# Kernel optimization log

Hardware: AMD Instinct MI355X
Metric: run time of the kernel (lower is better)

## Reference

```python
import jax, jax.numpy as jnp
import numpy as np

VX, VY = 0.16, 0.16
X_OFF = VX / 2 + 0.0          # vx/2 + point_cloud_range[0]
Y_OFF = VY / 2 + (-39.68)     # vy/2 + point_cloud_range[1]
BN_EPS = 1e-3


def setup_inputs() -> dict:
    key = jax.random.key(0)
    P, N, C_IN, C_OUT = 40000, 32, 9, 64
    k1, k2, k3, k4, k5, k6 = jax.random.split(key, 6)
    voxels = jax.random.normal(k1, (P, N, 4), dtype=jnp.float32)
    # at least 1 real point per pillar (avoids div-by-zero, matches real data)
    voxel_num_points = jax.random.randint(k2, (P,), 1, N + 1, dtype=jnp.int32)
    # coords layout: [batch_idx, z, y, x]
    voxel_coords = jax.random.randint(k3, (P, 4), 0, 432, dtype=jnp.int32)
    W = jax.random.normal(k4, (C_OUT, C_IN), dtype=jnp.float32) * 0.1  # 1x1 conv kernel
    gamma = jnp.ones((C_OUT,), jnp.float32)
    beta = jnp.zeros((C_OUT,), jnp.float32)
    running_mean = jax.random.normal(k5, (C_OUT,), jnp.float32) * 0.01
    running_var = jax.random.uniform(k6, (C_OUT,), jnp.float32, minval=0.5, maxval=1.5)
    return {
        "voxels": voxels,
        "W": W,
        "gamma": gamma,
        "beta": beta,
        "running_mean": running_mean,
        "running_var": running_var,
        "voxel_num_points": voxel_num_points,
        "voxel_coords": voxel_coords,
    }


def reference(voxels, W, gamma, beta, running_mean, running_var,
              voxel_num_points, voxel_coords):
    P, N, _ = voxels.shape
    npts = voxel_num_points.astype(voxels.dtype)[:, None, None]          # [P,1,1]
    points_mean = voxels[:, :, :3].sum(axis=1, keepdims=True) / npts     # [P,1,3]
    f_cluster = voxels[:, :, :3] - points_mean                           # [P,N,3]

    cx = voxel_coords[:, 3].astype(voxels.dtype)[:, None] * VX + X_OFF   # [P,1]
    cy = voxel_coords[:, 2].astype(voxels.dtype)[:, None] * VY + Y_OFF
    x_c = voxels[:, :, 0] - cx                                           # [P,N]
    y_c = voxels[:, :, 1] - cy

    # NOTE: torch code mutates features[:,:,:2] in place via the f_center view,
    # so the first two feature channels are ALSO the centered coordinates.
    feats = jnp.concatenate(
        [x_c[..., None], y_c[..., None], voxels[:, :, 2:4],
         f_cluster, x_c[..., None], y_c[..., None]], axis=-1)            # [P,N,9]

    mask = (jnp.arange(N)[None, :] < voxel_num_points[:, None]).astype(voxels.dtype)
    feats = feats * mask[..., None]

    # PFNLayer: 1x1 conv (no bias) + BatchNorm (eval) + ReLU + max over points
    x = jnp.einsum('pnc,oc->pno', feats, W)                              # [P,N,64]
    scale = gamma / jnp.sqrt(running_var + BN_EPS)
    x = (x - running_mean) * scale + beta
    x = jax.nn.relu(x)
    return x.max(axis=1)                                                 # [P,64] pillar_features
```

## Files before the change

### kernel.cpp

```cpp
#include <hip/hip_runtime.h>
#include <cstdint>


__global__ __launch_bounds__(64) void pillar_setup_kernel(
    const float* __restrict__ Wp,
    const float* __restrict__ gamma_p,
    const float* __restrict__ beta_p,
    const float* __restrict__ rmean_p,
    const float* __restrict__ rvar_p,
    float*       __restrict__ params)
{
    const int o = threadIdx.x;
    float w[9];
    #pragma unroll
    for (int c = 0; c < 9; ++c) w[c] = Wp[o * 9 + c];
    const float s = gamma_p[o] / sqrtf(rvar_p[o] + 1e-3f);

    params[0 * 64 + o] = (w[0] + w[4] + w[7]) * s;
    params[1 * 64 + o] = (w[1] + w[5] + w[8]) * s;
    params[2 * 64 + o] = (w[2] + w[6]) * s;
    params[3 * 64 + o] = w[3] * s;
    params[4 * 64 + o] = beta_p[o] - rmean_p[o] * s;
    params[5 * 64 + o] = (w[0] + w[7]) * s;
    params[6 * 64 + o] = (w[1] + w[8]) * s;
    params[7 * 64 + o] = w[4] * s;
    params[8 * 64 + o] = w[5] * s;
    params[9 * 64 + o] = w[6] * s;
}

__global__ __launch_bounds__(256) void pillar_vfe_kernel(
    const float4* __restrict__ voxels4,
    const float*  __restrict__ params,
    const int*    __restrict__ npts_p,
    const int*    __restrict__ coords_p,
    float*        __restrict__ out,
    int P)
{
    __shared__ float4 sh[4 * 32];

    const int tid    = threadIdx.x;
    const int pblock = blockIdx.x * 4;

    if (tid < 128) {
        const int gidx = pblock * 32 + tid;
        if (gidx < P * 32) sh[tid] = voxels4[gidx];
    }
    __syncthreads();

    const int wave = tid >> 6;
    const int lane = tid & 63;
    const int p    = pblock + wave;
    if (p >= P) return;

    const float A0   = params[0 * 64 + lane];
    const float A1   = params[1 * 64 + lane];
    const float A2   = params[2 * 64 + lane];
    const float A3   = params[3 * 64 + lane];
    const float C0   = params[4 * 64 + lane];
    const float SW07 = params[5 * 64 + lane];
    const float SW18 = params[6 * 64 + lane];
    const float SW4  = params[7 * 64 + lane];
    const float SW5  = params[8 * 64 + lane];
    const float SW6  = params[9 * 64 + lane];

    const int   npts = npts_p[p];
    const float fn   = (float)npts;
    const float cx   = (float)coords_p[p * 4 + 3] * 0.16f + 0.08f;
    const float cy   = (float)coords_p[p * 4 + 2] * 0.16f + (0.08f - 39.68f);

    const float4* shp = sh + wave * 32;

    float sx = 0.f, sy = 0.f, sz = 0.f;
    if (lane < 32) {
        const float4 v = shp[lane];
        sx = v.x; sy = v.y; sz = v.z;
    }
    #pragma unroll
    for (int m = 32; m >= 1; m >>= 1) {
        sx += __shfl_xor(sx, m, 64);
        sy += __shfl_xor(sy, m, 64);
        sz += __shfl_xor(sz, m, 64);
    }

    const float C1 = C0 - cx * SW07 - cy * SW18;
    float vmax = -3.4e38f;
    for (int n = 0; n < npts; ++n) {
        const float4 v = shp[n];
        float acc = C1;
        acc  = fmaf(v.x, A0, acc);
        acc  = fmaf(v.y, A1, acc);
        acc  = fmaf(v.z, A2, acc);
        acc  = fmaf(v.w, A3, acc);
        vmax = fmaxf(vmax, acc);
    }

    const float inv_n    = 1.0f / fn;
    const float meanterm = (sx * SW4 + sy * SW5 + sz * SW6) * inv_n;
    vmax -= meanterm;
    if (npts < 32) vmax = fmaxf(vmax, C0);
    out[p * 64 + lane] = fmaxf(vmax, 0.0f);
}

extern "C" void kernel_launch(void* const* d_in, const int* in_sizes, int n_in,
                              void* d_out, int out_size, void* d_ws, size_t ws_size,
                              hipStream_t stream) {
    const float4* voxels = (const float4*)d_in[0];
    const float*  W      = (const float*)d_in[1];
    const float*  gamma_ = (const float*)d_in[2];
    const float*  beta_  = (const float*)d_in[3];
    const float*  rmean  = (const float*)d_in[4];
    const float*  rvar   = (const float*)d_in[5];
    const int*    npts   = (const int*)d_in[6];
    const int*    coords = (const int*)d_in[7];
    float*        out    = (float*)d_out;
    float*        params = (float*)d_ws;

    const int P = in_sizes[6];

    pillar_setup_kernel<<<1, 64, 0, stream>>>(W, gamma_, beta_, rmean, rvar, params);

    const int blocks = (P + 3) / 4;
    pillar_vfe_kernel<<<blocks, 256, 0, stream>>>(voxels, params, npts, coords, out, P);
}
```

Before: 101.1 us.

## Fuse param setup into VFE kernel and process four pillars per wave

Drops the separate setup kernel launch and has each thread recompute the folded BN/conv coefficients from W, gamma, beta and the running stats. Each block now handles 16 pillars, with each wave looping over 4 of them so the coefficient cost is spread out, and the point loop is unrolled by two with separate max accumulators. The mean reduction uses a 32-wide shuffle on duplicated lanes. The trade-off is redundant per-thread parameter maths and more shared memory per block in exchange for one fewer launch and more work per wave.

```diff
diff --git a/kernel.cpp b/kernel.cpp
--- a/kernel.cpp
+++ b/kernel.cpp
@@ -2,103 +2,115 @@
 #include <cstdint>
 
 
-__global__ __launch_bounds__(64) void pillar_setup_kernel(
-    const float* __restrict__ Wp,
-    const float* __restrict__ gamma_p,
-    const float* __restrict__ beta_p,
-    const float* __restrict__ rmean_p,
-    const float* __restrict__ rvar_p,
-    float*       __restrict__ params)
-{
-    const int o = threadIdx.x;
-    float w[9];
-    #pragma unroll
-    for (int c = 0; c < 9; ++c) w[c] = Wp[o * 9 + c];
-    const float s = gamma_p[o] / sqrtf(rvar_p[o] + 1e-3f);
+#define PPB 16
+#define PPW 4
 
-    params[0 * 64 + o] = (w[0] + w[4] + w[7]) * s;
-    params[1 * 64 + o] = (w[1] + w[5] + w[8]) * s;
-    params[2 * 64 + o] = (w[2] + w[6]) * s;
-    params[3 * 64 + o] = w[3] * s;
-    params[4 * 64 + o] = beta_p[o] - rmean_p[o] * s;
-    params[5 * 64 + o] = (w[0] + w[7]) * s;
-    params[6 * 64 + o] = (w[1] + w[8]) * s;
-    params[7 * 64 + o] = w[4] * s;
-    params[8 * 64 + o] = w[5] * s;
-    params[9 * 64 + o] = w[6] * s;
-}
-
-__global__ __launch_bounds__(256) void pillar_vfe_kernel(
+__global__ __launch_bounds__(256) void pillar_vfe_fused(
     const float4* __restrict__ voxels4,
-    const float*  __restrict__ params,
+    const float*  __restrict__ Wp,
+    const float*  __restrict__ gamma_p,
+    const float*  __restrict__ beta_p,
+    const float*  __restrict__ rmean_p,
+    const float*  __restrict__ rvar_p,
     const int*    __restrict__ npts_p,
     const int*    __restrict__ coords_p,
     float*        __restrict__ out,
     int P)
 {
-    __shared__ float4 sh[4 * 32];
+    __shared__ float4 sh[PPB * 32];
 
     const int tid    = threadIdx.x;
-    const int pblock = blockIdx.x * 4;
+    const int pblock = blockIdx.x * PPB;
 
-    if (tid < 128) {
-        const int gidx = pblock * 32 + tid;
-        if (gidx < P * 32) sh[tid] = voxels4[gidx];
+    {
+        const int base = pblock * 32;
+        #pragma unroll
+        for (int r = 0; r < (PPB * 32) / 256; ++r) {
+            const int i = tid + r * 256;
+            const int g = base + i;
+            if (g < P * 32) sh[i] = voxels4[g];
+        }
     }
+
+    const int lane = tid & 63;
+    float w[9];
+    #pragma unroll
+    for (int c = 0; c < 9; ++c) w[c] = Wp[lane * 9 + c];
+    const float s    = gamma_p[lane] / sqrtf(rvar_p[lane] + 1e-3f);
+    const float A0   = (w[0] + w[4] + w[7]) * s;
+    const float A1   = (w[1] + w[5] + w[8]) * s;
+    const float A2   = (w[2] + w[6]) * s;
+    const float A3   = w[3] * s;
+    const float C0   = beta_p[lane] - rmean_p[lane] * s;
+    const float SW07 = (w[0] + w[7]) * s;
+    const float SW18 = (w[1] + w[8]) * s;
+    const float SW4  = w[4] * s;
+    const float SW5  = w[5] * s;
+    const float SW6  = w[6] * s;
+
+    const int wave  = tid >> 6;
+    const int pbase = pblock + wave * PPW;
+
+    int   npts[PPW];
+    float cx[PPW], cy[PPW];
+    #pragma unroll
+    for (int g2 = 0; g2 < PPW; ++g2) {
+        const int p = min(pbase + g2, P - 1);
+        npts[g2] = npts_p[p];
+        cx[g2]   = (float)coords_p[p * 4 + 3] * 0.16f + 0.08f;
+        cy[g2]   = (float)coords_p[p * 4 + 2] * 0.16f + (0.08f - 39.68f);
+    }
+
     __syncthreads();
 
-    const int wave = tid >> 6;
-    const int lane = tid & 63;
-    const int p    = pblock + wave;
-    if (p >= P) return;
+    #pragma unroll
+    for (int g2 = 0; g2 < PPW; ++g2) {
+        const int p = pbase + g2;
+        if (p >= P) break;
+        const float4* shp = sh + (wave * PPW + g2) * 32;
 
-    const float A0   = params[0 * 64 + lane];
-    const float A1   = params[1 * 64 + lane];
-    const float A2   = params[2 * 64 + lane];
-    const float A3   = params[3 * 64 + lane];
-    const float C0   = params[4 * 64 + lane];
-    const float SW07 = params[5 * 64 + lane];
-    const float SW18 = params[6 * 64 + lane];
-    const float SW4  = params[7 * 64 + lane];
-    const float SW5  = params[8 * 64 + lane];
-    const float SW6  = params[9 * 64 + lane];
+        const float4 vm = shp[lane & 31];
+        float sx = vm.x, sy = vm.y, sz = vm.z;
+        #pragma unroll
+        for (int m = 16; m >= 1; m >>= 1) {
+            sx += __shfl_xor(sx, m, 64);
+            sy += __shfl_xor(sy, m, 64);
+            sz += __shfl_xor(sz, m, 64);
+        }
 
-    const int   npts = npts_p[p];
-    const float fn   = (float)npts;
-    const float cx   = (float)coords_p[p * 4 + 3] * 0.16f + 0.08f;
-    const float cy   = (float)coords_p[p * 4 + 2] * 0.16f + (0.08f - 39.68f);
+        const int   n_pts = npts[g2];
+        const float C1    = C0 - cx[g2] * SW07 - cy[g2] * SW18;
 
-    const float4* shp = sh + wave * 32;
+        float vmax0 = -3.4e38f, vmax1 = -3.4e38f;
+        int n = 0;
+        for (; n + 2 <= n_pts; n += 2) {
+            const float4 va = shp[n];
+            const float4 vb = shp[n + 1];
+            float a = C1, b = C1;
+            a = fmaf(va.x, A0, a);  b = fmaf(vb.x, A0, b);
+            a = fmaf(va.y, A1, a);  b = fmaf(vb.y, A1, b);
+            a = fmaf(va.z, A2, a);  b = fmaf(vb.z, A2, b);
+            a = fmaf(va.w, A3, a);  b = fmaf(vb.w, A3, b);
+            vmax0 = fmaxf(vmax0, a);
+            vmax1 = fmaxf(vmax1, b);
+        }
+        if (n < n_pts) {
+            const float4 va = shp[n];
+            float a = C1;
+            a = fmaf(va.x, A0, a);
+            a = fmaf(va.y, A1, a);
+            a = fmaf(va.z, A2, a);
+            a = fmaf(va.w, A3, a);
+            vmax0 = fmaxf(vmax0, a);
+        }
+        float vmax = fmaxf(vmax0, vmax1);
 
-    float sx = 0.f, sy = 0.f, sz = 0.f;
-    if (lane < 32) {
-        const float4 v = shp[lane];
-        sx = v.x; sy = v.y; sz = v.z;
+        const float inv_n    = 1.0f / (float)n_pts;
+        const float meanterm = (sx * SW4 + sy * SW5 + sz * SW6) * inv_n;
+        vmax -= meanterm;
+        if (n_pts < 32) vmax = fmaxf(vmax, C0);
+        out[p * 64 + lane] = fmaxf(vmax, 0.0f);
     }
-    #pragma unroll
-    for (int m = 32; m >= 1; m >>= 1) {
-        sx += __shfl_xor(sx, m, 64);
-        sy += __shfl_xor(sy, m, 64);
-        sz += __shfl_xor(sz, m, 64);
-    }
-
-    const float C1 = C0 - cx * SW07 - cy * SW18;
-    float vmax = -3.4e38f;
-    for (int n = 0; n < npts; ++n) {
-        const float4 v = shp[n];
-        float acc = C1;
-        acc  = fmaf(v.x, A0, acc);
-        acc  = fmaf(v.y, A1, acc);
-        acc  = fmaf(v.z, A2, acc);
-        acc  = fmaf(v.w, A3, acc);
-        vmax = fmaxf(vmax, acc);
-    }
-
-    const float inv_n    = 1.0f / fn;
-    const float meanterm = (sx * SW4 + sy * SW5 + sz * SW6) * inv_n;
-    vmax -= meanterm;
-    if (npts < 32) vmax = fmaxf(vmax, C0);
-    out[p * 64 + lane] = fmaxf(vmax, 0.0f);
 }
 
 extern "C" void kernel_launch(void* const* d_in, const int* in_sizes, int n_in,
@@ -113,12 +125,10 @@
     const int*    npts   = (const int*)d_in[6];
     const int*    coords = (const int*)d_in[7];
     float*        out    = (float*)d_out;
-    float*        params = (float*)d_ws;
 
     const int P = in_sizes[6];
 
-    pillar_setup_kernel<<<1, 64, 0, stream>>>(W, gamma_, beta_, rmean, rvar, params);
-
-    const int blocks = (P + 3) / 4;
-    pillar_vfe_kernel<<<blocks, 256, 0, stream>>>(voxels, params, npts, coords, out, P);
+    const int blocks = (P + PPB - 1) / PPB;
+    pillar_vfe_fused<<<blocks, 256, 0, stream>>>(
+        voxels, W, gamma_, beta_, rmean, rvar, npts, coords, out, P);
 }
```

Measured after the change: 93.90 us. -7.1%, faster.
